# Kernel optimization log

Hardware: AMD Instinct MI355X
Metric: run time of the kernel (lower is better)

The kernel has to match this reference:

```python
import jax, jax.numpy as jnp
import numpy as np

N = 40000      # nodes
E = 640000     # edges (avg degree 16)
D = 128        # feature dim (in_features == all hidden_dims due to residual)


def setup_inputs() -> dict:
    key = jax.random.key(0)
    ks = jax.random.split(key, 8)
    xavier = (6.0 / (D + D)) ** 0.5
    return {
        "x": jax.random.normal(ks[0], (N, D), dtype=jnp.float32),
        "edge_index": jax.random.randint(ks[1], (2, E), 0, N, dtype=jnp.int64),
        "W_t": jax.random.uniform(ks[2], (D, D), jnp.float32, -xavier, xavier),
        "b_t": jnp.zeros((D,), jnp.float32),
        "W0": jax.random.uniform(ks[3], (D, D), jnp.float32, -xavier, xavier),
        "b0": jnp.zeros((D,), jnp.float32),
        "W1": jax.random.uniform(ks[4], (D, D), jnp.float32, -xavier, xavier),
        "b1": jnp.zeros((D,), jnp.float32),
    }


def _gcn_layer(h, row, col, W, b):
    # linear transform, then edge-wise gather + scatter-add aggregation
    z = jnp.matmul(h, W)                                  # [N, D]
    agg = jnp.zeros_like(z).at[row].add(z[col])           # out[row] += z[col]
    return jax.nn.relu(agg + b)


def reference(x, edge_index, W_t, b_t, W0, b0, W1, b1):
    row, col = edge_index[0], edge_index[1]
    h = jnp.matmul(x, W_t) + b_t                          # self.transform
    # residual GCN layers (dropout p=0.0 -> identity; eval mode)
    h = h + _gcn_layer(h, row, col, W0, b0)
    h = h + _gcn_layer(h, row, col, W1, b1)
    return h
```

## Files before the change

### kernel.cpp

```cpp
#include <hip/hip_runtime.h>
#include <hip/hip_bf16.h>

#define N_NODES 40000
#define N_EDGES 640000
#define DIM     128
#define NB      157
#define GEMMB   625
#define HEB     1250
#define CHUNKS  64
#define CHUNK_E 10000
#define LDSW    10000

typedef __attribute__((ext_vector_type(8))) short short8;
typedef __attribute__((ext_vector_type(4))) float f32x4;
typedef __attribute__((ext_vector_type(2))) float f32x2;

__device__ inline short f2bf(float f) {
    __hip_bfloat16 h = __float2bfloat16(f);
    return *reinterpret_cast<short*>(&h);
}
__device__ inline float bf2f(short u) {
    union { unsigned int i; float f; } x;
    x.i = ((unsigned int)(unsigned short)u) << 16;
    return x.f;
}

__device__ inline int fragidx(int k, int n) {
    int kb = k >> 5, kq = (k >> 3) & 3, j = k & 7;
    int nt = n >> 4, nl = n & 15;
    return (((kb * 8 + nt) * 64 + kq * 16 + nl) * 8 + j);
}

__global__ __launch_bounds__(256) void prep_zero(const float* __restrict__ Wt,
                                                 const float* __restrict__ W0,
                                                 const float* __restrict__ W1,
                                                 const float* __restrict__ bt,
                                                 short* __restrict__ WtF,
                                                 short* __restrict__ WfF,
                                                 short* __restrict__ W1F,
                                                 float* __restrict__ btf,
                                                 int* __restrict__ flagtot) {
    int b = blockIdx.x;
    if (b < 64) {
        int gid = b * 256 + threadIdx.x;
        int k = gid >> 7, n = gid & 127;
        float wf = 0.f;
        for (int kk = 0; kk < 128; ++kk)
            wf += Wt[k * 128 + kk] * W0[kk * 128 + n];
        int fi = fragidx(k, n);
        WtF[fi] = f2bf(Wt[k * 128 + n]);
        W1F[fi] = f2bf(W1[k * 128 + n]);
        WfF[fi] = f2bf(wf);
        if (gid < 128) {
            float s = 0.f;
            for (int kk = 0; kk < 128; ++kk) s += bt[kk] * W0[kk * 128 + n];
            btf[n] = s;
        }
    } else {
        flagtot[threadIdx.x]       = 0;
        flagtot[threadIdx.x + 256] = 0;
    }
}

__global__ __launch_bounds__(256) void histlds_gemm(const int* __restrict__ rows,
                                                    unsigned char* __restrict__ rank8,
                                                    unsigned int* __restrict__ cnt8w,
                                                    const float* __restrict__ A,
                                                    const short* __restrict__ WtF,
                                                    const short* __restrict__ WfF,
                                                    const float* __restrict__ bt,
                                                    const float* __restrict__ btf,
                                                    float* __restrict__ H,
                                                    __hip_bfloat16* __restrict__ Z) {
    __shared__ unsigned int lcnt[LDSW];

    if (blockIdx.x < CHUNKS) {
        for (int i = threadIdx.x; i < LDSW; i += 256) lcnt[i] = 0u;
        __syncthreads();
        const int base = blockIdx.x * CHUNK_E;
#pragma unroll
        for (int i = 0; i < 40; ++i) {
            int o = i * 256 + threadIdx.x;
            if (o < CHUNK_E) {
                int e = base + o;
                int r = rows[e];
                unsigned int sh = (unsigned int)(r & 3) * 8u;
                unsigned int old = atomicAdd(&lcnt[r >> 2], 1u << sh);
                rank8[e] = (unsigned char)((old >> sh) & 0xFFu);
            }
        }
        __syncthreads();
        unsigned int* out = cnt8w + blockIdx.x * LDSW;
        for (int i = threadIdx.x; i < LDSW; i += 256) out[i] = lcnt[i];
        return;
    }

    const int t    = threadIdx.x;
    const int wave = t >> 6;
    const int l    = t & 63;
    const int nl   = l & 15;
    const int quad = l >> 4;
    const int wRow = (blockIdx.x - CHUNKS) * 64 + wave * 16;

    f32x4 accH[8], accZ[8];
#pragma unroll
    for (int nt = 0; nt < 8; ++nt) {
        accH[nt] = (f32x4){0.f, 0.f, 0.f, 0.f};
        accZ[nt] = (f32x4){0.f, 0.f, 0.f, 0.f};
    }

#pragma unroll
    for (int kb = 0; kb < 4; ++kb) {
        const float* ap = A + (size_t)(wRow + nl) * 128 + kb * 32 + quad * 8;
        float4 f0 = *(const float4*)ap;
        float4 f1 = *(const float4*)(ap + 4);
        short8 afrag;
        afrag[0] = f2bf(f0.x); afrag[1] = f2bf(f0.y);
        afrag[2] = f2bf(f0.z); afrag[3] = f2bf(f0.w);
        afrag[4] = f2bf(f1.x); afrag[5] = f2bf(f1.y);
        afrag[6] = f2bf(f1.z); afrag[7] = f2bf(f1.w);
#pragma unroll
        for (int nt = 0; nt < 8; ++nt) {
            int off = ((kb * 8 + nt) * 64 + l) * 8;
            short8 bt_frag = *(const short8*)&WtF[off];
            short8 bf_frag = *(const short8*)&WfF[off];
            accH[nt] = __builtin_amdgcn_mfma_f32_16x16x32_bf16(afrag, bt_frag, accH[nt], 0, 0, 0);
            accZ[nt] = __builtin_amdgcn_mfma_f32_16x16x32_bf16(afrag, bf_frag, accZ[nt], 0, 0, 0);
        }
    }

#pragma unroll
    for (int nt = 0; nt < 8; ++nt) {
        int col = nt * 16 + nl;
        float bH = bt[col];
        float bZ = btf[col];
#pragma unroll
        for (int r = 0; r < 4; ++r) {
            int row = wRow + quad * 4 + r;
            H[(size_t)row * 128 + col] = accH[nt][r] + bH;
            *(short*)&Z[(size_t)row * 128 + col] = f2bf(accZ[nt][r] + bZ);
        }
    }
}

__global__ __launch_bounds__(256) void scan_onepass(unsigned char* __restrict__ cnt8,
                                                    int* __restrict__ flags,
                                                    int* __restrict__ totals,
                                                    int* __restrict__ row_ptr) {
    __shared__ int sh[256];
    const int b = blockIdx.x;
    const int t = threadIdx.x;
    const int i = b * 256 + t;

    int deg = 0;
    if (i < N_NODES) {
#pragma unroll 8
        for (int c = 0; c < CHUNKS; ++c) deg += cnt8[(size_t)c * N_NODES + i];
    }

    int val = deg;
    sh[t] = val;
    __syncthreads();
    for (int off = 1; off < 256; off <<= 1) {
        int a = (t >= off) ? sh[t - off] : 0;
        __syncthreads();
        val += a;
        sh[t] = val;
        __syncthreads();
    }
    const int excl  = val - deg;
    const int total = sh[255];

    if (t == 0) {
        atomicExch(&totals[b], total);
        __threadfence();
        atomicExch(&flags[b], 1);
    }

    int v = 0;
    if (t < NB) {
        while (atomicAdd(&flags[t], 0) == 0) { }
        v = atomicAdd(&totals[t], 0);
    }
    __syncthreads();
    int val2 = v;
    sh[t] = val2;
    __syncthreads();
    for (int off = 1; off < 256; off <<= 1) {
        int a = (t >= off) ? sh[t - off] : 0;
        __syncthreads();
        val2 += a;
        sh[t] = val2;
        __syncthreads();
    }
    int blkOff = (b == 0) ? 0 : sh[b - 1];

    if (i < N_NODES) {
        int base = excl + blkOff;
        row_ptr[i] = base;
        int run = 0;
#pragma unroll 8
        for (int c = 0; c < CHUNKS; ++c) {
            int cv = cnt8[(size_t)c * N_NODES + i];
            cnt8[(size_t)c * N_NODES + i] = (unsigned char)run;
            run += cv;
        }
    }
    if (i == 0) row_ptr[N_NODES] = N_EDGES;
}

__global__ __launch_bounds__(256) void scatter_plain(const int* __restrict__ rows,
                                                     const int* __restrict__ cols,
                                                     const unsigned char* __restrict__ rank8,
                                                     const unsigned char* __restrict__ pref8,
                                                     const int* __restrict__ row_ptr,
                                                     unsigned short* __restrict__ adj) {
    int gid = blockIdx.x * 256 + threadIdx.x;
#pragma unroll
    for (int h = 0; h < 2; ++h) {
        int e = gid + h * HEB * 256;
        int r = rows[e];
        int c = e / CHUNK_E;
        int pos = row_ptr[r] + (int)pref8[(size_t)c * N_NODES + r] + (int)rank8[e];
        adj[pos] = (unsigned short)cols[e];
    }
}

__global__ __launch_bounds__(256) void agg0_gemm(const __hip_bfloat16* __restrict__ z0,
                                                 const int* __restrict__ row_ptr,
                                                 const unsigned short* __restrict__ adj,
                                                 const float* __restrict__ bias,
                                                 const short* __restrict__ W1F,
                                                 float* __restrict__ H,
                                                 unsigned char* __restrict__ Z1) {
    __shared__ short hs[16][136];

    const int t    = threadIdx.x;
    const int wave = t >> 6;
    const int l    = t & 63;
    const int quad = l >> 4;
    const int sl   = l & 15;
    const int nodeBase = blockIdx.x * 16;

#pragma unroll
    for (int u = 0; u < 4; ++u) {
        const int m    = wave * 4 + u;
        const int node = nodeBase + m;
        const int s = row_ptr[node];
        const int e = row_ptr[node + 1];

        float acc[8];
#pragma unroll
        for (int j = 0; j < 8; ++j) acc[j] = 0.f;

        int it = s + quad;
        for (; it + 12 < e; it += 16) {
            int c0 = adj[it];
            int c1 = adj[it + 4];
            int c2 = adj[it + 8];
            int c3 = adj[it + 12];
            short8 v0 = *(const short8*)&z0[(size_t)c0 * DIM + sl * 8];
            short8 v1 = *(const short8*)&z0[(size_t)c1 * DIM + sl * 8];
            short8 v2 = *(const short8*)&z0[(size_t)c2 * DIM + sl * 8];
            short8 v3 = *(const short8*)&z0[(size_t)c3 * DIM + sl * 8];
#pragma unroll
            for (int j = 0; j < 8; ++j)
                acc[j] += (bf2f(v0[j]) + bf2f(v1[j])) + (bf2f(v2[j]) + bf2f(v3[j]));
        }
        for (; it + 4 < e; it += 8) {
            int c0 = adj[it];
            int c1 = adj[it + 4];
            short8 v0 = *(const short8*)&z0[(size_t)c0 * DIM + sl * 8];
            short8 v1 = *(const short8*)&z0[(size_t)c1 * DIM + sl * 8];
#pragma unroll
            for (int j = 0; j < 8; ++j) acc[j] += bf2f(v0[j]) + bf2f(v1[j]);
        }
        if (it < e) {
            int c = adj[it];
            short8 v = *(const short8*)&z0[(size_t)c * DIM + sl * 8];
#pragma unroll
            for (int j = 0; j < 8; ++j) acc[j] += bf2f(v[j]);
        }

#pragma unroll
        for (int j = 0; j < 8; ++j) acc[j] += __shfl_xor(acc[j], 16, 64);
#pragma unroll
        for (int j = 0; j < 8; ++j) acc[j] += __shfl_xor(acc[j], 32, 64);

        if (quad == 0) {
            float* hp = H + (size_t)node * DIM + sl * 8;
            float4 h0 = *(float4*)hp;
            float4 h1 = *(float4*)(hp + 4);
            float4 b0v = *(const float4*)&bias[sl * 8];
            float4 b1v = *(const float4*)&bias[sl * 8 + 4];
            float r[8];
            r[0] = acc[0] + b0v.x; r[1] = acc[1] + b0v.y; r[2] = acc[2] + b0v.z; r[3] = acc[3] + b0v.w;
            r[4] = acc[4] + b1v.x; r[5] = acc[5] + b1v.y; r[6] = acc[6] + b1v.z; r[7] = acc[7] + b1v.w;
            float hn[8];
            hn[0] = h0.x; hn[1] = h0.y; hn[2] = h0.z; hn[3] = h0.w;
            hn[4] = h1.x; hn[5] = h1.y; hn[6] = h1.z; hn[7] = h1.w;
            short8 o;
#pragma unroll
            for (int j = 0; j < 8; ++j) {
                float rr = r[j] > 0.f ? r[j] : 0.f;
                hn[j] += rr;
                o[j] = f2bf(hn[j]);
            }
            *(float4*)hp       = make_float4(hn[0], hn[1], hn[2], hn[3]);
            *(float4*)(hp + 4) = make_float4(hn[4], hn[5], hn[6], hn[7]);
            *(short8*)&hs[m][sl * 8] = o;
        }
    }
    __syncthreads();

    f32x4 acc2[2];
    acc2[0] = (f32x4){0.f, 0.f, 0.f, 0.f};
    acc2[1] = (f32x4){0.f, 0.f, 0.f, 0.f};
#pragma unroll
    for (int kb = 0; kb < 4; ++kb) {
        short8 afrag = *(const short8*)&hs[sl][kb * 32 + quad * 8];
#pragma unroll
        for (int nt2 = 0; nt2 < 2; ++nt2) {
            int nt = wave * 2 + nt2;
            short8 bfrag = *(const short8*)&W1F[((kb * 8 + nt) * 64 + l) * 8];
            acc2[nt2] = __builtin_amdgcn_mfma_f32_16x16x32_bf16(afrag, bfrag, acc2[nt2], 0, 0, 0);
        }
    }
#pragma unroll
    for (int nt2 = 0; nt2 < 2; ++nt2) {
        int col = (wave * 2 + nt2) * 16 + sl;
#pragma unroll
        for (int r = 0; r < 4; ++r) {
            int row = nodeBase + quad * 4 + r;
            float v = acc2[nt2][r];
            int packed = __builtin_amdgcn_cvt_pk_fp8_f32(v, v, 0, false);
            Z1[(size_t)row * 128 + col] = (unsigned char)(packed & 0xFF);
        }
    }
}

__global__ __launch_bounds__(256) void agg_final(const unsigned char* __restrict__ z1,
                                                 const int* __restrict__ row_ptr,
                                                 const unsigned short* __restrict__ adj,
                                                 const float* __restrict__ bias,
                                                 float* __restrict__ H) {
    const int wave = threadIdx.x >> 6;
    const int l    = threadIdx.x & 63;
    const int quad = l >> 4;
    const int sl   = l & 15;
    const int node = blockIdx.x * 4 + wave;
    if (node >= N_NODES) return;

    const int s = row_ptr[node];
    const int e = row_ptr[node + 1];

    float acc[8];
#pragma unroll
    for (int j = 0; j < 8; ++j) acc[j] = 0.f;

#define ADD_FP8(u2)                                                          \
    {                                                                        \
        f32x2 a0 = __builtin_amdgcn_cvt_pk_f32_fp8((u2).x, false);           \
        f32x2 a1 = __builtin_amdgcn_cvt_pk_f32_fp8((u2).x, true);            \
        f32x2 a2 = __builtin_amdgcn_cvt_pk_f32_fp8((u2).y, false);           \
        f32x2 a3 = __builtin_amdgcn_cvt_pk_f32_fp8((u2).y, true);            \
        acc[0] += a0.x; acc[1] += a0.y; acc[2] += a1.x; acc[3] += a1.y;      \
        acc[4] += a2.x; acc[5] += a2.y; acc[6] += a3.x; acc[7] += a3.y;      \
    }

    int it = s + quad;
    for (; it + 12 < e; it += 16) {
        int c0 = adj[it];
        int c1 = adj[it + 4];
        int c2 = adj[it + 8];
        int c3 = adj[it + 12];
        uint2 v0 = *(const uint2*)&z1[(size_t)c0 * 128 + sl * 8];
        uint2 v1 = *(const uint2*)&z1[(size_t)c1 * 128 + sl * 8];
        uint2 v2 = *(const uint2*)&z1[(size_t)c2 * 128 + sl * 8];
        uint2 v3 = *(const uint2*)&z1[(size_t)c3 * 128 + sl * 8];
        ADD_FP8(v0); ADD_FP8(v1); ADD_FP8(v2); ADD_FP8(v3);
    }
    for (; it + 4 < e; it += 8) {
        int c0 = adj[it];
        int c1 = adj[it + 4];
        uint2 v0 = *(const uint2*)&z1[(size_t)c0 * 128 + sl * 8];
        uint2 v1 = *(const uint2*)&z1[(size_t)c1 * 128 + sl * 8];
        ADD_FP8(v0); ADD_FP8(v1);
    }
    if (it < e) {
        int c = adj[it];
        uint2 v = *(const uint2*)&z1[(size_t)c * 128 + sl * 8];
        ADD_FP8(v);
    }
#undef ADD_FP8

#pragma unroll
    for (int j = 0; j < 8; ++j) acc[j] += __shfl_xor(acc[j], 16, 64);
#pragma unroll
    for (int j = 0; j < 8; ++j) acc[j] += __shfl_xor(acc[j], 32, 64);

    if (quad == 0) {
        float* hp = H + (size_t)node * DIM + sl * 8;
        float4 h0 = *(float4*)hp;
        float4 h1 = *(float4*)(hp + 4);
        float4 b0 = *(const float4*)&bias[sl * 8];
        float4 b1 = *(const float4*)&bias[sl * 8 + 4];
        float r0 = acc[0] + b0.x, r1 = acc[1] + b0.y, r2 = acc[2] + b0.z, r3 = acc[3] + b0.w;
        float r4 = acc[4] + b1.x, r5 = acc[5] + b1.y, r6 = acc[6] + b1.z, r7 = acc[7] + b1.w;
        h0.x += r0 > 0.f ? r0 : 0.f;  h0.y += r1 > 0.f ? r1 : 0.f;
        h0.z += r2 > 0.f ? r2 : 0.f;  h0.w += r3 > 0.f ? r3 : 0.f;
        h1.x += r4 > 0.f ? r4 : 0.f;  h1.y += r5 > 0.f ? r5 : 0.f;
        h1.z += r6 > 0.f ? r6 : 0.f;  h1.w += r7 > 0.f ? r7 : 0.f;
        *(float4*)hp       = h0;
        *(float4*)(hp + 4) = h1;
    }
}

extern "C" void kernel_launch(void* const* d_in, const int* in_sizes, int n_in,
                              void* d_out, int out_size, void* d_ws, size_t ws_size,
                              hipStream_t stream) {
    const float* x   = (const float*)d_in[0];
    const int*   ei  = (const int*)d_in[1];
    const float* W_t = (const float*)d_in[2];
    const float* b_t = (const float*)d_in[3];
    const float* W0  = (const float*)d_in[4];
    const float* b0  = (const float*)d_in[5];
    const float* W1  = (const float*)d_in[6];
    const float* b1  = (const float*)d_in[7];

    const int* rows = ei;
    const int* cols = ei + N_EDGES;

    float* H = (float*)d_out;

    char* w = (char*)d_ws;
    __hip_bfloat16* Z0 = (__hip_bfloat16*)w;  w += (size_t)N_NODES * DIM * 2;
    unsigned char*  Z1 = (unsigned char*)w;   w += (size_t)N_NODES * DIM;
    short* WtF = (short*)w;  w += 128 * 128 * 2;
    short* WfF = (short*)w;  w += 128 * 128 * 2;
    short* W1F = (short*)w;  w += 128 * 128 * 2;
    float* btf = (float*)w;  w += 128 * 4;
    int* row_ptr = (int*)w;  w += (N_NODES + 1) * 4;
    int* flags   = (int*)w;  w += 256 * 4;
    int* totals  = (int*)w;  w += 256 * 4;
    unsigned int* cnt8w = (unsigned int*)w;  w += (size_t)CHUNKS * LDSW * 4;
    unsigned char* rank8 = (unsigned char*)w;  w += (size_t)N_EDGES;
    unsigned short* adj  = (unsigned short*)w;

    const int aggBlocks = (N_NODES + 3) / 4;

    prep_zero<<<65, 256, 0, stream>>>(W_t, W0, W1, b_t, WtF, WfF, W1F, btf, flags);

    histlds_gemm<<<CHUNKS + GEMMB, 256, 0, stream>>>(rows, rank8, cnt8w,
                                                     x, WtF, WfF, b_t, btf, H, Z0);

    scan_onepass<<<NB, 256, 0, stream>>>((unsigned char*)cnt8w, flags, totals, row_ptr);

    scatter_plain<<<HEB, 256, 0, stream>>>(rows, cols, rank8, (unsigned char*)cnt8w,
                                           row_ptr, adj);

    agg0_gemm<<<N_NODES / 16, 256, 0, stream>>>(Z0, row_ptr, adj, b0, W1F, H, Z1);

    agg_final<<<aggBlocks, 256, 0, stream>>>(Z1, row_ptr, adj, b1, H);
}
```

Baseline: 186.9 us.

## Merge launches: histogram into prep, scan+GEMM+scatter into one kernel

The edge histogram moves into the weight-prep kernel. The decoupled scan, the transform GEMM and the CSR scatter are merged into a single launch, and scatter blocks spin on a done counter until all scan blocks finish. This cuts two kernel launches and lets the GEMM blocks overlap the scan and scatter phases. The cost is a spin-wait dependency that assumes all scan blocks become resident before the scatter blocks, and it adds an extra zeroed counter.

Result: slower. 332.4 us (+77.9%).

```diff
diff --git a/kernel.cpp b/kernel.cpp
--- a/kernel.cpp
+++ b/kernel.cpp
@@ -11,6 +11,10 @@
 #define CHUNK_E 10000
 #define LDSW    10000
 
+#define HIST0   65
+#define GEMM0   NB
+#define SCAT0   (NB + GEMMB)
+
 typedef __attribute__((ext_vector_type(8))) short short8;
 typedef __attribute__((ext_vector_type(4))) float f32x4;
 typedef __attribute__((ext_vector_type(2))) float f32x2;
@@ -31,16 +35,21 @@
     return (((kb * 8 + nt) * 64 + kq * 16 + nl) * 8 + j);
 }
 
-__global__ __launch_bounds__(256) void prep_zero(const float* __restrict__ Wt,
-                                                 const float* __restrict__ W0,
-                                                 const float* __restrict__ W1,
-                                                 const float* __restrict__ bt,
-                                                 short* __restrict__ WtF,
-                                                 short* __restrict__ WfF,
-                                                 short* __restrict__ W1F,
-                                                 float* __restrict__ btf,
-                                                 int* __restrict__ flagtot) {
-    int b = blockIdx.x;
+__global__ __launch_bounds__(256) void prep_hist_zero(const float* __restrict__ Wt,
+                                                      const float* __restrict__ W0,
+                                                      const float* __restrict__ W1,
+                                                      const float* __restrict__ bt,
+                                                      short* __restrict__ WtF,
+                                                      short* __restrict__ WfF,
+                                                      short* __restrict__ W1F,
+                                                      float* __restrict__ btf,
+                                                      int* __restrict__ flagtot,
+                                                      const int* __restrict__ rows,
+                                                      unsigned char* __restrict__ rank8,
+                                                      unsigned int* __restrict__ cnt8w) {
+    __shared__ unsigned int lcnt[LDSW];
+    const int b = blockIdx.x;
+
     if (b < 64) {
         int gid = b * 256 + threadIdx.x;
         int k = gid >> 7, n = gid & 127;
@@ -56,28 +65,14 @@
             for (int kk = 0; kk < 128; ++kk) s += bt[kk] * W0[kk * 128 + n];
             btf[n] = s;
         }
-    } else {
+    } else if (b == 64) {
         flagtot[threadIdx.x]       = 0;
         flagtot[threadIdx.x + 256] = 0;
-    }
-}
-
-__global__ __launch_bounds__(256) void histlds_gemm(const int* __restrict__ rows,
-                                                    unsigned char* __restrict__ rank8,
-                                                    unsigned int* __restrict__ cnt8w,
-                                                    const float* __restrict__ A,
-                                                    const short* __restrict__ WtF,
-                                                    const short* __restrict__ WfF,
-                                                    const float* __restrict__ bt,
-                                                    const float* __restrict__ btf,
-                                                    float* __restrict__ H,
-                                                    __hip_bfloat16* __restrict__ Z) {
-    __shared__ unsigned int lcnt[LDSW];
-
-    if (blockIdx.x < CHUNKS) {
+        flagtot[threadIdx.x + 512] = 0;
+    } else {
         for (int i = threadIdx.x; i < LDSW; i += 256) lcnt[i] = 0u;
         __syncthreads();
-        const int base = blockIdx.x * CHUNK_E;
+        const int base = (b - HIST0) * CHUNK_E;
 #pragma unroll
         for (int i = 0; i < 40; ++i) {
             int o = i * 256 + threadIdx.x;
@@ -90,138 +85,160 @@
             }
         }
         __syncthreads();
-        unsigned int* out = cnt8w + blockIdx.x * LDSW;
+        unsigned int* out = cnt8w + (size_t)(b - HIST0) * LDSW;
         for (int i = threadIdx.x; i < LDSW; i += 256) out[i] = lcnt[i];
+    }
+}
+
+__global__ __launch_bounds__(256) void scan_gemm_scatter(unsigned char* __restrict__ cnt8,
+                                                         int* __restrict__ flags,
+                                                         int* __restrict__ totals,
+                                                         int* __restrict__ done,
+                                                         int* __restrict__ row_ptr,
+                                                         const float* __restrict__ A,
+                                                         const short* __restrict__ WtF,
+                                                         const short* __restrict__ WfF,
+                                                         const float* __restrict__ bt,
+                                                         const float* __restrict__ btf,
+                                                         float* __restrict__ H,
+                                                         __hip_bfloat16* __restrict__ Z,
+                                                         const int* __restrict__ rows,
+                                                         const int* __restrict__ cols,
+                                                         const unsigned char* __restrict__ rank8,
+                                                         unsigned short* __restrict__ adj) {
+    __shared__ int sh[256];
+    const int blk = blockIdx.x;
+    const int t   = threadIdx.x;
+
+    if (blk < NB) {
+        const int b = blk;
+        const int i = b * 256 + t;
+
+        int deg = 0;
+        if (i < N_NODES) {
+#pragma unroll 8
+            for (int c = 0; c < CHUNKS; ++c) deg += cnt8[(size_t)c * N_NODES + i];
+        }
+
+        int val = deg;
+        sh[t] = val;
+        __syncthreads();
+        for (int off = 1; off < 256; off <<= 1) {
+            int a = (t >= off) ? sh[t - off] : 0;
+            __syncthreads();
+            val += a;
+            sh[t] = val;
+            __syncthreads();
+        }
+        const int excl  = val - deg;
+        const int total = sh[255];
+
+        if (t == 0) {
+            atomicExch(&totals[b], total);
+            __threadfence();
+            atomicExch(&flags[b], 1);
+        }
+
+        int v = 0;
+        if (t < NB) {
+            while (atomicAdd(&flags[t], 0) == 0) { }
+            v = atomicAdd(&totals[t], 0);
+        }
+        __syncthreads();
+        int val2 = v;
+        sh[t] = val2;
+        __syncthreads();
+        for (int off = 1; off < 256; off <<= 1) {
+            int a = (t >= off) ? sh[t - off] : 0;
+            __syncthreads();
+            val2 += a;
+            sh[t] = val2;
+            __syncthreads();
+        }
+        int blkOff = (b == 0) ? 0 : sh[b - 1];
+
+        if (i < N_NODES) {
+            int base = excl + blkOff;
+            row_ptr[i] = base;
+            int run = 0;
+#pragma unroll 8
+            for (int c = 0; c < CHUNKS; ++c) {
+                int cv = cnt8[(size_t)c * N_NODES + i];
+                cnt8[(size_t)c * N_NODES + i] = (unsigned char)run;
+                run += cv;
+            }
+        }
+        if (i == 0) row_ptr[N_NODES] = N_EDGES;
+
+        __threadfence();
+        __syncthreads();
+        if (t == 0) atomicAdd(done, 1);
         return;
     }
 
-    const int t    = threadIdx.x;
-    const int wave = t >> 6;
-    const int l    = t & 63;
-    const int nl   = l & 15;
-    const int quad = l >> 4;
-    const int wRow = (blockIdx.x - CHUNKS) * 64 + wave * 16;
-
-    f32x4 accH[8], accZ[8];
-#pragma unroll
-    for (int nt = 0; nt < 8; ++nt) {
-        accH[nt] = (f32x4){0.f, 0.f, 0.f, 0.f};
-        accZ[nt] = (f32x4){0.f, 0.f, 0.f, 0.f};
-    }
-
-#pragma unroll
-    for (int kb = 0; kb < 4; ++kb) {
-        const float* ap = A + (size_t)(wRow + nl) * 128 + kb * 32 + quad * 8;
-        float4 f0 = *(const float4*)ap;
-        float4 f1 = *(const float4*)(ap + 4);
-        short8 afrag;
-        afrag[0] = f2bf(f0.x); afrag[1] = f2bf(f0.y);
-        afrag[2] = f2bf(f0.z); afrag[3] = f2bf(f0.w);
-        afrag[4] = f2bf(f1.x); afrag[5] = f2bf(f1.y);
-        afrag[6] = f2bf(f1.z); afrag[7] = f2bf(f1.w);
+    if (blk < SCAT0) {
+        const int wave = t >> 6;
+        const int l    = t & 63;
+        const int nl   = l & 15;
+        const int quad = l >> 4;
+        const int wRow = (blk - GEMM0) * 64 + wave * 16;
+
+        f32x4 accH[8], accZ[8];
 #pragma unroll
         for (int nt = 0; nt < 8; ++nt) {
-            int off = ((kb * 8 + nt) * 64 + l) * 8;
-            short8 bt_frag = *(const short8*)&WtF[off];
-            short8 bf_frag = *(const short8*)&WfF[off];
-            accH[nt] = __builtin_amdgcn_mfma_f32_16x16x32_bf16(afrag, bt_frag, accH[nt], 0, 0, 0);
-            accZ[nt] = __builtin_amdgcn_mfma_f32_16x16x32_bf16(afrag, bf_frag, accZ[nt], 0, 0, 0);
-        }
-    }
-
-#pragma unroll
-    for (int nt = 0; nt < 8; ++nt) {
-        int col = nt * 16 + nl;
-        float bH = bt[col];
-        float bZ = btf[col];
-#pragma unroll
-        for (int r = 0; r < 4; ++r) {
-            int row = wRow + quad * 4 + r;
-            H[(size_t)row * 128 + col] = accH[nt][r] + bH;
-            *(short*)&Z[(size_t)row * 128 + col] = f2bf(accZ[nt][r] + bZ);
-        }
-    }
-}
-
-__global__ __launch_bounds__(256) void scan_onepass(unsigned char* __restrict__ cnt8,
-                                                    int* __restrict__ flags,
-                                                    int* __restrict__ totals,
-                                                    int* __restrict__ row_ptr) {
-    __shared__ int sh[256];
-    const int b = blockIdx.x;
-    const int t = threadIdx.x;
-    const int i = b * 256 + t;
-
-    int deg = 0;
-    if (i < N_NODES) {
-#pragma unroll 8
-        for (int c = 0; c < CHUNKS; ++c) deg += cnt8[(size_t)c * N_NODES + i];
-    }
-
-    int val = deg;
-    sh[t] = val;
+            accH[nt] = (f32x4){0.f, 0.f, 0.f, 0.f};
+            accZ[nt] = (f32x4){0.f, 0.f, 0.f, 0.f};
+        }
+
+#pragma unroll
+        for (int kb = 0; kb < 4; ++kb) {
+            const float* ap = A + (size_t)(wRow + nl) * 128 + kb * 32 + quad * 8;
+            float4 f0 = *(const float4*)ap;
+            float4 f1 = *(const float4*)(ap + 4);
+            short8 afrag;
+            afrag[0] = f2bf(f0.x); afrag[1] = f2bf(f0.y);
+            afrag[2] = f2bf(f0.z); afrag[3] = f2bf(f0.w);
+            afrag[4] = f2bf(f1.x); afrag[5] = f2bf(f1.y);
+            afrag[6] = f2bf(f1.z); afrag[7] = f2bf(f1.w);
+#pragma unroll
+            for (int nt = 0; nt < 8; ++nt) {
+                int off = ((kb * 8 + nt) * 64 + l) * 8;
+                short8 bt_frag = *(const short8*)&WtF[off];
+                short8 bf_frag = *(const short8*)&WfF[off];
+                accH[nt] = __builtin_amdgcn_mfma_f32_16x16x32_bf16(afrag, bt_frag, accH[nt], 0, 0, 0);
+                accZ[nt] = __builtin_amdgcn_mfma_f32_16x16x32_bf16(afrag, bf_frag, accZ[nt], 0, 0, 0);
+            }
+        }
+
+#pragma unroll
+        for (int nt = 0; nt < 8; ++nt) {
+            int col = nt * 16 + nl;
+            float bH = bt[col];
+            float bZ = btf[col];
+#pragma unroll
+            for (int r = 0; r < 4; ++r) {
+                int row = wRow + quad * 4 + r;
+                H[(size_t)row * 128 + col] = accH[nt][r] + bH;
+                *(short*)&Z[(size_t)row * 128 + col] = f2bf(accZ[nt][r] + bZ);
+            }
+        }
+        return;
+    }
+
+    if (t == 0) {
+        while (__hip_atomic_load(done, __ATOMIC_RELAXED, __HIP_MEMORY_SCOPE_AGENT) < NB)
+            __builtin_amdgcn_s_sleep(8);
+    }
     __syncthreads();
-    for (int off = 1; off < 256; off <<= 1) {
-        int a = (t >= off) ? sh[t - off] : 0;
-        __syncthreads();
-        val += a;
-        sh[t] = val;
-        __syncthreads();
-    }
-    const int excl  = val - deg;
-    const int total = sh[255];
-
-    if (t == 0) {
-        atomicExch(&totals[b], total);
-        __threadfence();
-        atomicExch(&flags[b], 1);
-    }
-
-    int v = 0;
-    if (t < NB) {
-        while (atomicAdd(&flags[t], 0) == 0) { }
-        v = atomicAdd(&totals[t], 0);
-    }
-    __syncthreads();
-    int val2 = v;
-    sh[t] = val2;
-    __syncthreads();
-    for (int off = 1; off < 256; off <<= 1) {
-        int a = (t >= off) ? sh[t - off] : 0;
-        __syncthreads();
-        val2 += a;
-        sh[t] = val2;
-        __syncthreads();
-    }
-    int blkOff = (b == 0) ? 0 : sh[b - 1];
-
-    if (i < N_NODES) {
-        int base = excl + blkOff;
-        row_ptr[i] = base;
-        int run = 0;
-#pragma unroll 8
-        for (int c = 0; c < CHUNKS; ++c) {
-            int cv = cnt8[(size_t)c * N_NODES + i];
-            cnt8[(size_t)c * N_NODES + i] = (unsigned char)run;
-            run += cv;
-        }
-    }
-    if (i == 0) row_ptr[N_NODES] = N_EDGES;
-}
-
-__global__ __launch_bounds__(256) void scatter_plain(const int* __restrict__ rows,
-                                                     const int* __restrict__ cols,
-                                                     const unsigned char* __restrict__ rank8,
-                                                     const unsigned char* __restrict__ pref8,
-                                                     const int* __restrict__ row_ptr,
-                                                     unsigned short* __restrict__ adj) {
-    int gid = blockIdx.x * 256 + threadIdx.x;
+    __threadfence();
+
+    int gid = (blk - SCAT0) * 256 + t;
 #pragma unroll
     for (int h = 0; h < 2; ++h) {
         int e = gid + h * HEB * 256;
         int r = rows[e];
         int c = e / CHUNK_E;
-        int pos = row_ptr[r] + (int)pref8[(size_t)c * N_NODES + r] + (int)rank8[e];
+        int pos = row_ptr[r] + (int)cnt8[(size_t)c * N_NODES + r] + (int)rank8[e];
         adj[pos] = (unsigned short)cols[e];
     }
 }
@@ -441,23 +458,25 @@
     short* W1F = (short*)w;  w += 128 * 128 * 2;
     float* btf = (float*)w;  w += 128 * 4;
     int* row_ptr = (int*)w;  w += (N_NODES + 1) * 4;
-    int* flags   = (int*)w;  w += 256 * 4;
-    int* totals  = (int*)w;  w += 256 * 4;
+    int* flagtot = (int*)w;  w += 768 * 4;
     unsigned int* cnt8w = (unsigned int*)w;  w += (size_t)CHUNKS * LDSW * 4;
     unsigned char* rank8 = (unsigned char*)w;  w += (size_t)N_EDGES;
     unsigned short* adj  = (unsigned short*)w;
 
+    int* flags  = flagtot;
+    int* totals = flagtot + 256;
+    int* done   = flagtot + 512;
+
     const int aggBlocks = (N_NODES + 3) / 4;
 
-    prep_zero<<<65, 256, 0, stream>>>(W_t, W0, W1, b_t, WtF, WfF, W1F, btf, flags);
-
-    histlds_gemm<<<CHUNKS + GEMMB, 256, 0, stream>>>(rows, rank8, cnt8w,
-                                                     x, WtF, WfF, b_t, btf, H, Z0);
-
-    scan_onepass<<<NB, 256, 0, stream>>>((unsigned char*)cnt8w, flags, totals, row_ptr);
-
-    scatter_plain<<<HEB, 256, 0, stream>>>(rows, cols, rank8, (unsigned char*)cnt8w,
-                                           row_ptr, adj);
+    prep_hist_zero<<<HIST0 + CHUNKS, 256, 0, stream>>>(W_t, W0, W1, b_t,
+                                                       WtF, WfF, W1F, btf, flagtot,
+                                                       rows, rank8, cnt8w);
+
+    scan_gemm_scatter<<<SCAT0 + HEB, 256, 0, stream>>>((unsigned char*)cnt8w,
+                                                       flags, totals, done, row_ptr,
+                                                       x, WtF, WfF, b_t, btf, H, Z0,
+                                                       rows, cols, rank8, adj);
 
     agg0_gemm<<<N_NODES / 16, 256, 0, stream>>>(Z0, row_ptr, adj, b0, W1F, H, Z1);
 
```
